# Optimization experiments

Hardware: AMD Instinct MI355X
Metric: run time of the kernel (lower is better)

The kernel has to match this reference:

```python
import jax, jax.numpy as jnp
import numpy as np

B, S, D_IN = 2, 2048, 1024
EMBED, HEADS = 1024, 16
HEAD_DIM = EMBED // HEADS

def setup_inputs() -> dict:
    key = jax.random.key(0)
    k1, k2, k3 = jax.random.split(key, 3)
    # xavier_uniform bounds
    def xavier(k, shape):
        fan_in, fan_out = shape[1], shape[0]
        lim = jnp.sqrt(6.0 / (fan_in + fan_out))
        return jax.random.uniform(k, shape, jnp.float32, -lim, lim)
    x = jax.random.normal(k1, (B, S, D_IN), jnp.float32)
    qkv_w = xavier(k2, (3 * EMBED, D_IN))   # torch Linear weight layout [out, in]
    qkv_b = jnp.zeros((3 * EMBED,), jnp.float32)
    o_w = xavier(k3, (EMBED, EMBED))
    o_b = jnp.zeros((EMBED,), jnp.float32)
    return {"x": x, "qkv_w": qkv_w, "qkv_b": qkv_b, "o_w": o_w, "o_b": o_b}

def reference(x, qkv_w, qkv_b, o_w, o_b):
    Bq, Sq, _ = x.shape
    qkv = x @ qkv_w.T + qkv_b                       # [B,S,3E]
    qkv = qkv.reshape(Bq, Sq, HEADS, 3 * HEAD_DIM).transpose(0, 2, 1, 3)  # [B,H,S,3d]
    q, k, v = jnp.split(qkv, 3, axis=-1)            # each [B,H,S,d]
    scale = 1.0 / jnp.sqrt(jnp.asarray(HEAD_DIM, x.dtype))
    logits = jnp.einsum('bhqd,bhkd->bhqk', q, k) * scale
    attn = jax.nn.softmax(logits, axis=-1)
    vals = jnp.einsum('bhqk,bhkd->bhqd', attn, v)   # [B,H,S,d]
    vals = vals.transpose(0, 2, 1, 3).reshape(Bq, Sq, EMBED)
    return vals @ o_w.T + o_b
```

## Files before the change

kernel.cpp:

```cpp
#include <hip/hip_runtime.h>
#include <hip/hip_bf16.h>

#define B_    2
#define S_    2048
#define DIN   1024
#define EMB   1024
#define NH    16
#define HD    64
#define N3    3072
#define MROWS 4096
#define KVB   64
#define QBLK  128
#define NT    (S_ / KVB)

typedef short bf16x8 __attribute__((ext_vector_type(8)));
typedef float f32x4  __attribute__((ext_vector_type(4)));
typedef float f32x16 __attribute__((ext_vector_type(16)));
typedef unsigned short u16;
typedef u16 u16x8 __attribute__((ext_vector_type(8)));
typedef u16 u16x4 __attribute__((ext_vector_type(4)));
typedef unsigned int u32;

__device__ __forceinline__ u16 f2bf(float f) {
  union { float f; unsigned u; } x; x.f = f;
  unsigned r = x.u + 0x7fffu + ((x.u >> 16) & 1u);
  return (u16)(r >> 16);
}

__device__ __forceinline__ u32 cvtpk(float lo, float hi) {
  u32 r;
  asm("v_cvt_pk_bf16_f32 %0, %1, %2" : "=v"(r) : "v"(lo), "v"(hi));
  return r;
}

__device__ __forceinline__ void gload16(const void* g, void* l) {
  __builtin_amdgcn_global_load_lds(
      (const __attribute__((address_space(1))) unsigned int*)g,
      (__attribute__((address_space(3))) unsigned int*)l, 16, 0, 0);
}

#define BARRIER() do { asm volatile("" ::: "memory"); \
                       __builtin_amdgcn_s_barrier();  \
                       asm volatile("" ::: "memory"); } while (0)

__global__ void cast4(const float* __restrict__ in, u16* __restrict__ out, int n4) {
  const int i = blockIdx.x * 256 + threadIdx.x;
  if (i < n4) {
    const float4 v = ((const float4*)in)[i];
    u16x4 o;
    o[0] = f2bf(v.x); o[1] = f2bf(v.y); o[2] = f2bf(v.z); o[3] = f2bf(v.w);
    ((u16x4*)out)[i] = o;
  }
}

template<int EPI>
__global__ __launch_bounds__(256)
void gemm_bt(const u16* __restrict__ A, const u16* __restrict__ W,
             const float* __restrict__ bias, float* __restrict__ Cf,
             u16* __restrict__ Qb, u16* __restrict__ Kb, u16* __restrict__ VbT,
             int M, int N, int K) {
  __shared__ u16 Als[128 * 32];
  __shared__ u16 Bls[128 * 32];
  const int tid  = threadIdx.x;
  const int wave = tid >> 6, lane = tid & 63;
  const int lhi  = lane >> 4, llo = lane & 15;
  const int wr   = wave >> 1, wc = wave & 1;
  const int m0   = blockIdx.y * 128, n0 = blockIdx.x * 128;

  f32x4 acc[4][4];
#pragma unroll
  for (int m = 0; m < 4; ++m)
#pragma unroll
    for (int n = 0; n < 4; ++n) acc[m][n] = f32x4{0.f, 0.f, 0.f, 0.f};

  for (int k0 = 0; k0 < K; k0 += 32) {
#pragma unroll
    for (int i = 0; i < 2; ++i) {
      const int e   = (tid + i * 256) * 8;
      const int row = e >> 5, col = e & 31;
      gload16(A + (size_t)(m0 + row) * K + k0 + col, (char*)Als + wave * 1024 + i * 4096);
      gload16(W + (size_t)(n0 + row) * K + k0 + col, (char*)Bls + wave * 1024 + i * 4096);
    }
    __syncthreads();
    bf16x8 af[4], bfr[4];
#pragma unroll
    for (int m = 0; m < 4; ++m) af[m]  = *(const bf16x8*)&Als[(wr * 64 + m * 16 + llo) * 32 + lhi * 8];
#pragma unroll
    for (int n = 0; n < 4; ++n) bfr[n] = *(const bf16x8*)&Bls[(wc * 64 + n * 16 + llo) * 32 + lhi * 8];
#pragma unroll
    for (int m = 0; m < 4; ++m)
#pragma unroll
      for (int n = 0; n < 4; ++n)
        acc[m][n] = __builtin_amdgcn_mfma_f32_16x16x32_bf16(af[m], bfr[n], acc[m][n], 0, 0, 0);
    __syncthreads();
  }

#pragma unroll
  for (int n = 0; n < 4; ++n) {
    const int colb = n0 + wc * 64 + n * 16;
    const int gcol = colb + llo;
    const float bv = bias[gcol];
    if (EPI == 0) {
      const int h   = colb / 192;
      const int rr  = colb - h * 192;
      const int sec = rr >> 6;
      const int d   = (rr & 63) + llo;
#pragma unroll
      for (int m = 0; m < 4; ++m) {
        const int rowb = m0 + wr * 64 + m * 16 + lhi * 4;
        const int b = rowb >> 11, s0 = rowb & 2047;
        if (sec == 2) {
          u16x4 vv;
#pragma unroll
          for (int r = 0; r < 4; ++r) vv[r] = f2bf(acc[m][n][r] + bv);
          *(u16x4*)&VbT[((size_t)(b * NH + h) * HD + d) * S_ + s0] = vv;
        } else {
          u16* dst = (sec == 0) ? Qb : Kb;
          const float scl = (sec == 0) ? 0.18033688f : 1.0f;
#pragma unroll
          for (int r = 0; r < 4; ++r)
            dst[(((size_t)(b * NH + h) * S_ + s0 + r) << 6) + d] = f2bf((acc[m][n][r] + bv) * scl);
        }
      }
    } else {
#pragma unroll
      for (int m = 0; m < 4; ++m) {
        const int rowb = m0 + wr * 64 + m * 16 + lhi * 4;
#pragma unroll
        for (int r = 0; r < 4; ++r)
          Cf[(size_t)(rowb + r) * N + gcol] = acc[m][n][r] + bv;
      }
    }
  }
}

__global__ __launch_bounds__(256, 2)
void attn_fwd(const u16* __restrict__ Qb, const u16* __restrict__ Kb,
              const u16* __restrict__ VbT, u16* __restrict__ Obf) {
  __shared__ __align__(16) u16 Kls[4][KVB * HD];
  __shared__ __align__(16) u16 Vls[4][HD * KVB];
  __shared__ __align__(16) float sBc[4][32];
  const int tid  = threadIdx.x;
  const int wave = tid >> 6, lane = tid & 63;
  const int q    = lane & 31, hi = lane >> 5;
  const int bh   = blockIdx.y;
  const int q0   = blockIdx.x * QBLK;
  const size_t base  = (size_t)bh * S_ * HD;
  const size_t basev = (size_t)bh * HD * S_;

  const int qrow = q0 + wave * 32 + q;
  bf16x8 qf[4];
#pragma unroll
  for (int c = 0; c < 4; ++c)
    qf[c] = *(const bf16x8*)&Qb[base + (size_t)qrow * HD + c * 16 + hi * 8];

  const int srow = tid >> 3;
  const int xs   = (tid & 7) ^ (srow & 7);
  const u16* kSrc = Kb  + base  + (size_t)srow * HD + xs * 8;
  const u16* vSrc = VbT + basev + (size_t)srow * S_ + xs * 8;
  const int ldsW = wave * 1024;

  const int gq = 16 * (q >> 4) + 8 * ((q >> 2) & 1) + (q & 3) + 4 * ((q >> 3) & 1);
  int offK[2][4], offV[2][4];
#pragma unroll
  for (int b = 0; b < 2; ++b)
#pragma unroll
    for (int c = 0; c < 4; ++c) {
      offK[b][c] = (b * 32 + gq) * 128 + (((c * 2 + hi) ^ (gq & 7)) << 4);
      offV[b][c] = (b * 32 + q)  * 128 + (((c * 2 + hi) ^ (q  & 7)) << 4);
    }

  f32x16 o0, o1;
#pragma unroll
  for (int r = 0; r < 16; ++r) { o0[r] = 0.f; o1[r] = 0.f; }
  float m_run = -1e30f, lsum = 0.f;

  auto issue = [&](int t) {
#pragma unroll
    for (int p = 0; p < 2; ++p) {
      gload16(kSrc + (size_t)t * KVB * HD + (size_t)p * 32 * HD,
              (char*)Kls[t & 3] + p * 4096 + ldsW);
      gload16(vSrc + t * KVB + (size_t)p * 32 * S_,
              (char*)Vls[t & 3] + p * 4096 + ldsW);
    }
  };

  auto qk = [&](int t, f32x16& s0, f32x16& s1) {
    const char* Kt = (const char*)Kls[t & 3];
#pragma unroll
    for (int r = 0; r < 16; ++r) { s0[r] = 0.f; s1[r] = 0.f; }
#pragma unroll
    for (int c = 0; c < 4; ++c) {
      bf16x8 k0 = *(const bf16x8*)(Kt + offK[0][c]);
      bf16x8 k1 = *(const bf16x8*)(Kt + offK[1][c]);
      s0 = __builtin_amdgcn_mfma_f32_32x32x16_bf16(k0, qf[c], s0, 0, 0, 0);
      s1 = __builtin_amdgcn_mfma_f32_32x32x16_bf16(k1, qf[c], s1, 0, 0, 0);
    }
  };

  auto sm = [&](f32x16& s0, f32x16& s1, u32 (&dw0)[8], u32 (&dw1)[8]) {
    float tm[16];
#pragma unroll
    for (int r = 0; r < 16; ++r) tm[r] = fmaxf(s0[r], s1[r]);
#pragma unroll
    for (int st = 8; st >= 1; st >>= 1)
#pragma unroll
      for (int i = 0; i < 16; ++i) if (i < st) tm[i] = fmaxf(tm[i], tm[i + st]);
    const float pm = fmaxf(tm[0], __shfl_xor(tm[0], 32));

    if (__any(pm > m_run + 10.0f)) {
      const float mnew  = fmaxf(m_run, pm);
      const float alpha = exp2f(m_run - mnew);
      sBc[wave][q] = alpha;
      asm volatile("s_waitcnt lgkmcnt(0)" ::: "memory");
      f32x4 av[4];
#pragma unroll
      for (int g = 0; g < 4; ++g) av[g] = *(const f32x4*)&sBc[wave][hi * 4 + g * 8];
#pragma unroll
      for (int r = 0; r < 16; ++r) {
        const float f = av[r >> 2][r & 3];
        o0[r] *= f; o1[r] *= f;
      }
      lsum *= alpha;
      m_run = mnew;
    }

    float t0 = 0.f, t1 = 0.f, t2 = 0.f, t3 = 0.f;
#pragma unroll
    for (int j = 0; j < 8; ++j) {
      const float a0 = exp2f(s0[2 * j] - m_run), a1 = exp2f(s0[2 * j + 1] - m_run);
      const float b0 = exp2f(s1[2 * j] - m_run), b1 = exp2f(s1[2 * j + 1] - m_run);
      t0 += a0; t1 += a1; t2 += b0; t3 += b1;
      dw0[j] = cvtpk(a0, a1);
      dw1[j] = cvtpk(b0, b1);
    }
    float ts = (t0 + t1) + (t2 + t3);
    ts += __shfl_xor(ts, 32);
    lsum += ts;
  };

  auto pv = [&](int t, u32 (&dw0)[8], u32 (&dw1)[8]) {
    const char* Vt = (const char*)Vls[t & 3];
#pragma unroll
    for (int c = 0; c < 4; ++c) {
      union { u32 u[4]; bf16x8 v; } P;
      if (c == 0)      { P.u[0] = dw0[0]; P.u[1] = dw0[1]; P.u[2] = dw0[2]; P.u[3] = dw0[3]; }
      else if (c == 1) { P.u[0] = dw0[4]; P.u[1] = dw0[5]; P.u[2] = dw0[6]; P.u[3] = dw0[7]; }
      else if (c == 2) { P.u[0] = dw1[0]; P.u[1] = dw1[1]; P.u[2] = dw1[2]; P.u[3] = dw1[3]; }
      else             { P.u[0] = dw1[4]; P.u[1] = dw1[5]; P.u[2] = dw1[6]; P.u[3] = dw1[7]; }
      bf16x8 v0 = *(const bf16x8*)(Vt + offV[0][c]);
      bf16x8 v1 = *(const bf16x8*)(Vt + offV[1][c]);
      o0 = __builtin_amdgcn_mfma_f32_32x32x16_bf16(P.v, v0, o0, 0, 0, 0);
      o1 = __builtin_amdgcn_mfma_f32_32x32x16_bf16(P.v, v1, o1, 0, 0, 0);
    }
  };

  f32x16 sE0, sE1, sO0, sO1;
  u32 dwE0[8], dwE1[8], dwO0[8], dwO1[8];

  issue(0); issue(1);
  for (int p = 0; p < NT / 2 - 1; ++p) {
    issue(2 * p + 2); issue(2 * p + 3);
    asm volatile("s_waitcnt vmcnt(8)" ::: "memory");
    BARRIER();
    qk(2 * p,     sE0, sE1);
    qk(2 * p + 1, sO0, sO1);
    sm(sE0, sE1, dwE0, dwE1);
    pv(2 * p,     dwE0, dwE1);
    sm(sO0, sO1, dwO0, dwO1);
    pv(2 * p + 1, dwO0, dwO1);
    BARRIER();
  }
  asm volatile("s_waitcnt vmcnt(0)" ::: "memory");
  BARRIER();
  qk(NT - 2, sE0, sE1);
  qk(NT - 1, sO0, sO1);
  sm(sE0, sE1, dwE0, dwE1);
  pv(NT - 2, dwE0, dwE1);
  sm(sO0, sO1, dwO0, dwO1);
  pv(NT - 1, dwO0, dwO1);

  const float li = 1.0f / lsum;
  sBc[wave][q] = li;
  asm volatile("s_waitcnt lgkmcnt(0)" ::: "memory");
  f32x4 lv[4];
#pragma unroll
  for (int g = 0; g < 4; ++g) lv[g] = *(const f32x4*)&sBc[wave][hi * 4 + g * 8];
  const int b = bh >> 4, h = bh & 15;
#pragma unroll
  for (int r = 0; r < 16; ++r) {
    const int qg = q0 + wave * 32 + (r & 3) + 8 * (r >> 2) + 4 * hi;
    const float f = lv[r >> 2][r & 3];
    u16* dst = Obf + ((size_t)(b * S_ + qg) * NH + h) * HD;
    dst[q]      = f2bf(o0[r] * f);
    dst[32 + q] = f2bf(o1[r] * f);
  }
}

extern "C" void kernel_launch(void* const* d_in, const int* in_sizes, int n_in,
                              void* d_out, int out_size, void* d_ws, size_t ws_size,
                              hipStream_t stream) {
  const float* x     = (const float*)d_in[0];
  const float* qkv_w = (const float*)d_in[1];
  const float* qkv_b = (const float*)d_in[2];
  const float* o_w   = (const float*)d_in[3];
  const float* o_b   = (const float*)d_in[4];
  float* out = (float*)d_out;

  char* ws = (char*)d_ws;
  u16* xbf  = (u16*)(ws);
  u16* wqkv = (u16*)(ws + (8u  << 20));
  u16* wo   = (u16*)(ws + (14u << 20));
  u16* Qb   = (u16*)(ws + (16u << 20));
  u16* Kb   = (u16*)(ws + (24u << 20));
  u16* VbT  = (u16*)(ws + (32u << 20));
  u16* atnb = xbf;

  cast4<<<4096, 256, 0, stream>>>(x,     xbf,  1048576);
  cast4<<<3072, 256, 0, stream>>>(qkv_w, wqkv,  786432);
  cast4<<<1024, 256, 0, stream>>>(o_w,   wo,    262144);

  gemm_bt<0><<<dim3(N3 / 128, MROWS / 128), 256, 0, stream>>>(
      xbf, wqkv, qkv_b, nullptr, Qb, Kb, VbT, MROWS, N3, DIN);

  attn_fwd<<<dim3(S_ / QBLK, B_ * NH), 256, 0, stream>>>(Qb, Kb, VbT, atnb);

  gemm_bt<1><<<dim3(EMB / 128, MROWS / 128), 256, 0, stream>>>(
      atnb, wo, o_b, out, nullptr, nullptr, nullptr, MROWS, EMB, EMB);
}
```

Measured before the change: 144.0 us.

## Double-buffer GEMM K-loop, fuse cast kernels, and drop QK accumulator zeroing

The three fp32-to-bf16 cast launches become a single kernel that picks its source by index range. The GEMM K loop double-buffers its LDS tiles, prefetching the next K slice with partial vmcnt waits so loads overlap the MFMAs. In attention, the first QK MFMA now accumulates into a constant zero vector instead of zeroing the score registers each tile. Together these aim to cut launch overhead, exposed global-load latency and a few VALU instructions, at the cost of doubled GEMM LDS use and a hand-tuned waitcnt that must match the number of outstanding loads.

```diff
diff --git a/kernel.cpp b/kernel.cpp
--- a/kernel.cpp
+++ b/kernel.cpp
@@ -43,14 +43,19 @@
                        __builtin_amdgcn_s_barrier();  \
                        asm volatile("" ::: "memory"); } while (0)
 
-__global__ void cast4(const float* __restrict__ in, u16* __restrict__ out, int n4) {
+__global__ __launch_bounds__(256)
+void cast_all(const float* __restrict__ x, const float* __restrict__ w1,
+              const float* __restrict__ w2, u16* __restrict__ ox,
+              u16* __restrict__ ow1, u16* __restrict__ ow2) {
   const int i = blockIdx.x * 256 + threadIdx.x;
-  if (i < n4) {
-    const float4 v = ((const float4*)in)[i];
-    u16x4 o;
-    o[0] = f2bf(v.x); o[1] = f2bf(v.y); o[2] = f2bf(v.z); o[3] = f2bf(v.w);
-    ((u16x4*)out)[i] = o;
-  }
+  const float* src; u16* dst; int off;
+  if (i < 1048576)              { src = x;  dst = ox;  off = i; }
+  else if (i < 1048576 + 786432){ src = w1; dst = ow1; off = i - 1048576; }
+  else                          { src = w2; dst = ow2; off = i - 1835008; }
+  const float4 v = ((const float4*)src)[off];
+  u16x4 o;
+  o[0] = f2bf(v.x); o[1] = f2bf(v.y); o[2] = f2bf(v.z); o[3] = f2bf(v.w);
+  ((u16x4*)dst)[off] = o;
 }
 
 template<int EPI>
@@ -59,13 +64,14 @@
              const float* __restrict__ bias, float* __restrict__ Cf,
              u16* __restrict__ Qb, u16* __restrict__ Kb, u16* __restrict__ VbT,
              int M, int N, int K) {
-  __shared__ u16 Als[128 * 32];
-  __shared__ u16 Bls[128 * 32];
+  __shared__ u16 Als[2][128 * 32];
+  __shared__ u16 Bls[2][128 * 32];
   const int tid  = threadIdx.x;
   const int wave = tid >> 6, lane = tid & 63;
   const int lhi  = lane >> 4, llo = lane & 15;
   const int wr   = wave >> 1, wc = wave & 1;
   const int m0   = blockIdx.y * 128, n0 = blockIdx.x * 128;
+  const int KT   = K >> 5;
 
   f32x4 acc[4][4];
 #pragma unroll
@@ -73,26 +79,40 @@
 #pragma unroll
     for (int n = 0; n < 4; ++n) acc[m][n] = f32x4{0.f, 0.f, 0.f, 0.f};
 
-  for (int k0 = 0; k0 < K; k0 += 32) {
+  auto issue = [&](int t) {
 #pragma unroll
     for (int i = 0; i < 2; ++i) {
       const int e   = (tid + i * 256) * 8;
       const int row = e >> 5, col = e & 31;
-      gload16(A + (size_t)(m0 + row) * K + k0 + col, (char*)Als + wave * 1024 + i * 4096);
-      gload16(W + (size_t)(n0 + row) * K + k0 + col, (char*)Bls + wave * 1024 + i * 4096);
-    }
-    __syncthreads();
+      gload16(A + (size_t)(m0 + row) * K + t * 32 + col,
+              (char*)Als[t & 1] + wave * 1024 + i * 4096);
+      gload16(W + (size_t)(n0 + row) * K + t * 32 + col,
+              (char*)Bls[t & 1] + wave * 1024 + i * 4096);
+    }
+  };
+
+  issue(0);
+  for (int t = 0; t < KT; ++t) {
+    if (t + 1 < KT) {
+      issue(t + 1);
+      asm volatile("s_waitcnt vmcnt(4)" ::: "memory");
+    } else {
+      asm volatile("s_waitcnt vmcnt(0)" ::: "memory");
+    }
+    BARRIER();
+    const u16* Ab = Als[t & 1];
+    const u16* Bb = Bls[t & 1];
     bf16x8 af[4], bfr[4];
 #pragma unroll
-    for (int m = 0; m < 4; ++m) af[m]  = *(const bf16x8*)&Als[(wr * 64 + m * 16 + llo) * 32 + lhi * 8];
-#pragma unroll
-    for (int n = 0; n < 4; ++n) bfr[n] = *(const bf16x8*)&Bls[(wc * 64 + n * 16 + llo) * 32 + lhi * 8];
+    for (int m = 0; m < 4; ++m) af[m]  = *(const bf16x8*)&Ab[(wr * 64 + m * 16 + llo) * 32 + lhi * 8];
+#pragma unroll
+    for (int n = 0; n < 4; ++n) bfr[n] = *(const bf16x8*)&Bb[(wc * 64 + n * 16 + llo) * 32 + lhi * 8];
 #pragma unroll
     for (int m = 0; m < 4; ++m)
 #pragma unroll
       for (int n = 0; n < 4; ++n)
         acc[m][n] = __builtin_amdgcn_mfma_f32_16x16x32_bf16(af[m], bfr[n], acc[m][n], 0, 0, 0);
-    __syncthreads();
+    BARRIER();
   }
 
 #pragma unroll
@@ -170,9 +190,9 @@
       offV[b][c] = (b * 32 + q)  * 128 + (((c * 2 + hi) ^ (q  & 7)) << 4);
     }
 
-  f32x16 o0, o1;
-#pragma unroll
-  for (int r = 0; r < 16; ++r) { o0[r] = 0.f; o1[r] = 0.f; }
+  f32x16 o0, o1, z16;
+#pragma unroll
+  for (int r = 0; r < 16; ++r) { o0[r] = 0.f; o1[r] = 0.f; z16[r] = 0.f; }
   float m_run = -1e30f, lsum = 0.f;
 
   auto issue = [&](int t) {
@@ -187,10 +207,14 @@
 
   auto qk = [&](int t, f32x16& s0, f32x16& s1) {
     const char* Kt = (const char*)Kls[t & 3];
-#pragma unroll
-    for (int r = 0; r < 16; ++r) { s0[r] = 0.f; s1[r] = 0.f; }
-#pragma unroll
-    for (int c = 0; c < 4; ++c) {
+    {
+      bf16x8 k0 = *(const bf16x8*)(Kt + offK[0][0]);
+      bf16x8 k1 = *(const bf16x8*)(Kt + offK[1][0]);
+      s0 = __builtin_amdgcn_mfma_f32_32x32x16_bf16(k0, qf[0], z16, 0, 0, 0);
+      s1 = __builtin_amdgcn_mfma_f32_32x32x16_bf16(k1, qf[0], z16, 0, 0, 0);
+    }
+#pragma unroll
+    for (int c = 1; c < 4; ++c) {
       bf16x8 k0 = *(const bf16x8*)(Kt + offK[0][c]);
       bf16x8 k1 = *(const bf16x8*)(Kt + offK[1][c]);
       s0 = __builtin_amdgcn_mfma_f32_32x32x16_bf16(k0, qf[c], s0, 0, 0, 0);
@@ -316,9 +340,7 @@
   u16* VbT  = (u16*)(ws + (32u << 20));
   u16* atnb = xbf;
 
-  cast4<<<4096, 256, 0, stream>>>(x,     xbf,  1048576);
-  cast4<<<3072, 256, 0, stream>>>(qkv_w, wqkv,  786432);
-  cast4<<<1024, 256, 0, stream>>>(o_w,   wo,    262144);
+  cast_all<<<8192, 256, 0, stream>>>(x, qkv_w, o_w, xbf, wqkv, wo);
 
   gemm_bt<0><<<dim3(N3 / 128, MROWS / 128), 256, 0, stream>>>(
       xbf, wqkv, qkv_b, nullptr, Qb, Kb, VbT, MROWS, N3, DIN);
```

After: 132.6 us. 7.9% less time.
